# Optimization experiments

Hardware: AMD Instinct MI355X
Metric: run time of the kernel (lower is better)

The kernel has to match this reference:

```python
import jax, jax.numpy as jnp
import numpy as np

B, S, D = 16, 1024, 512
H = 2048
E = 16
TOP_K = 4


def setup_inputs() -> dict:
    key = jax.random.key(0)
    ks = jax.random.split(key, 8)
    scale = 0.02
    x = jax.random.normal(ks[0], (B, S, D), dtype=jnp.float32)
    router_w = jax.random.normal(ks[1], (D, E), dtype=jnp.float32) * scale
    router_b = jax.random.normal(ks[2], (E,), dtype=jnp.float32) * scale
    w1 = jax.random.normal(ks[3], (E, D, H), dtype=jnp.float32) * scale
    b1 = jax.random.normal(ks[4], (E, H), dtype=jnp.float32) * scale
    w2 = jax.random.normal(ks[5], (E, H, D), dtype=jnp.float32) * scale
    b2 = jax.random.normal(ks[6], (E, D), dtype=jnp.float32) * scale
    return {"x": x, "router_w": router_w, "router_b": router_b,
            "w1": w1, "b1": b1, "w2": w2, "b2": b2}


def reference(x, router_w, router_b, w1, b1, w2, b2):
    # x: [B, S, D] -> flatten tokens
    x_flat = x.reshape(-1, D)                       # [T, D]
    logits = x_flat @ router_w + router_b           # [T, E]
    top_vals, top_idx = jax.lax.top_k(logits, TOP_K)  # [T, K]
    gates = jax.nn.softmax(top_vals, axis=-1)       # softmax over selected experts only
    # Combined per-expert gate weight per token: sum over k slots routed to e.
    onehot = jax.nn.one_hot(top_idx, E, dtype=x.dtype)  # [T, K, E]
    comb = jnp.einsum('tk,tke->te', gates, onehot)      # [T, E]
    out = jnp.zeros_like(x_flat)
    for e in range(E):  # fixed small expert count
        h = jax.nn.relu(x_flat @ w1[e] + b1[e])     # [T, H]
        y = h @ w2[e] + b2[e]                       # [T, D]
        out = out + comb[:, e:e + 1] * y
    return out.reshape(x.shape)
```

## Files before the change

kernel.cpp:

```cpp
#include <hip/hip_runtime.h>
#include <stdint.h>

#define T_TOK 16384
#define DIM 512
#define HID 2048
#define NE 16
#define TOPK 4
#define BM 256
#define BN 256
#define BKT 64
#define PAIR_CAP 69632
#define MAX_TILES 272
#define NB_CNT 64
#define QOFF 2080

typedef short s8v __attribute__((ext_vector_type(8)));
typedef float f4v __attribute__((ext_vector_type(4)));
typedef unsigned int u4v __attribute__((ext_vector_type(4)));

__device__ __forceinline__ unsigned short f2bf(float f) {
  unsigned int u = __builtin_bit_cast(unsigned int, f);
  u = (u + 0x7fffu + ((u >> 16) & 1u)) >> 16;
  return (unsigned short)u;
}
__device__ __forceinline__ float bf2f(unsigned short h) {
  return __builtin_bit_cast(float, (unsigned int)h << 16);
}

__device__ __forceinline__ void gload16(const void* g, void* l) {
  __builtin_amdgcn_global_load_lds(
      (const __attribute__((address_space(1))) unsigned int*)(uintptr_t)g,
      (__attribute__((address_space(3))) unsigned int*)(uintptr_t)l,
      16, 0, 0);
}

__global__ __launch_bounds__(256) void k_transpose_cast(const float* __restrict__ src,
                                                        unsigned short* __restrict__ dst,
                                                        int R, int C) {
  __shared__ float tile[32][33];
  size_t zo = (size_t)blockIdx.z * R * C;
  src += zo; dst += zo;
  int c0 = blockIdx.x * 32, r0 = blockIdx.y * 32;
  int tx = threadIdx.x, ty = threadIdx.y;
#pragma unroll
  for (int i = 0; i < 4; ++i)
    tile[ty + 8 * i][tx] = src[(size_t)(r0 + ty + 8 * i) * C + c0 + tx];
  __syncthreads();
#pragma unroll
  for (int i = 0; i < 4; ++i)
    dst[(size_t)(c0 + ty + 8 * i) * R + r0 + tx] = f2bf(tile[tx][ty + 8 * i]);
}

__global__ __launch_bounds__(256) void k_router(const float* __restrict__ x,
                                                const float* __restrict__ rw,
                                                const float* __restrict__ rb,
                                                int* __restrict__ topki,
                                                float* __restrict__ topkg,
                                                unsigned short* __restrict__ xb) {
  int wv = threadIdx.x >> 6, lane = threadIdx.x & 63;
  int t = blockIdx.x * 4 + wv;
  const float* xr = x + (size_t)t * DIM;
  unsigned short* xbr = xb + (size_t)t * DIM;
  double acc[NE];
#pragma unroll
  for (int e = 0; e < NE; ++e) acc[e] = 0.0;
  for (int it = 0; it < DIM / 64; ++it) {
    float xv = xr[it * 64 + lane];
    xbr[it * 64 + lane] = f2bf(xv);
    const float* r = rw + (size_t)(it * 64 + lane) * NE;
#pragma unroll
    for (int e = 0; e < NE; ++e) acc[e] += (double)xv * (double)r[e];
  }
#pragma unroll
  for (int off = 32; off >= 1; off >>= 1) {
#pragma unroll
    for (int e = 0; e < NE; ++e) acc[e] += __shfl_xor(acc[e], off, 64);
  }
  if (lane == 0) {
    float v[NE];
#pragma unroll
    for (int e = 0; e < NE; ++e) v[e] = (float)acc[e] + rb[e];
    int idx[TOPK]; float val[TOPK];
#pragma unroll
    for (int k = 0; k < TOPK; ++k) {
      float best = -1e30f; int bi = 0;
#pragma unroll
      for (int e = 0; e < NE; ++e)
        if (v[e] > best) { best = v[e]; bi = e; }
      idx[k] = bi; val[k] = best; v[bi] = -1e30f;
    }
    float m = val[0], s = 0.f, g[TOPK];
#pragma unroll
    for (int k = 0; k < TOPK; ++k) { g[k] = __expf(val[k] - m); s += g[k]; }
    float inv = 1.f / s;
#pragma unroll
    for (int k = 0; k < TOPK; ++k) {
      topki[t * TOPK + k] = idx[k];
      topkg[t * TOPK + k] = g[k] * inv;
    }
  }
}

__global__ __launch_bounds__(256) void k_count(const int* __restrict__ topki,
                                               int* __restrict__ meta) {
  __shared__ int lcnt[NE];
  int tid = threadIdx.x;
  if (tid < NE) lcnt[tid] = 0;
  __syncthreads();
  int base = blockIdx.x * 1024 + tid * 4;
#pragma unroll
  for (int j = 0; j < 4; ++j) atomicAdd(&lcnt[topki[base + j]], 1);
  __syncthreads();
  if (tid < NE) meta[1056 + blockIdx.x * NE + tid] = lcnt[tid];
}

__global__ __launch_bounds__(256) void k_plan(int* __restrict__ meta,
                                              int* __restrict__ ptok,
                                              float* __restrict__ pgate) {
  __shared__ int cnt_s[NE], po_s[NE + 1];
  int tid = threadIdx.x;
  for (int i = tid; i < 1024; i += 256) meta[QOFF + i] = 0;
  if (tid < NE) {
    int s = 0;
    for (int b = 0; b < NB_CNT; ++b) s += meta[1056 + b * NE + tid];
    cnt_s[tid] = s;
  }
  __syncthreads();
  if (tid == 0) {
    int off = 0;
    for (int e = 0; e < NE; ++e) {
      po_s[e] = off;
      meta[1 + e] = off;
      off += ((cnt_s[e] + BM - 1) / BM) * BM;
    }
    po_s[NE] = off;
    meta[1 + NE] = off;
    meta[0] = off / BM;
  }
  __syncthreads();
  if (tid < NE) {
    int run = po_s[tid];
    for (int b = 0; b < NB_CNT; ++b) {
      meta[32 + b * NE + tid] = run;
      run += meta[1056 + b * NE + tid];
    }
  }
  for (int e = 0; e < NE; ++e) {
    int start = po_s[e] + cnt_s[e], end = po_s[e + 1];
    for (int i = start + tid; i < end; i += 256) { ptok[i] = 0; pgate[i] = 0.f; }
  }
}

__global__ __launch_bounds__(256) void k_scatter(const int* __restrict__ topki,
                                                 const float* __restrict__ topkg,
                                                 const int* __restrict__ meta,
                                                 int* __restrict__ ptok,
                                                 float* __restrict__ pgate,
                                                 int* __restrict__ sinv) {
  __shared__ int lcnt[NE];
  int tid = threadIdx.x;
  if (tid < NE) lcnt[tid] = 0;
  __syncthreads();
  int base = blockIdx.x * 1024 + tid * 4;
#pragma unroll
  for (int j = 0; j < 4; ++j) {
    int i = base + j;
    int e = topki[i];
    int r = atomicAdd(&lcnt[e], 1);
    int slot = meta[32 + blockIdx.x * NE + e] + r;
    ptok[slot] = i >> 2;
    pgate[slot] = topkg[i];
    sinv[i] = slot;
  }
}


#define EBAR() asm volatile("s_barrier" ::: "memory")
#define SP1() __builtin_amdgcn_s_setprio(1)
#define SP0() __builtin_amdgcn_s_setprio(0)
#define VMC(n) asm volatile("s_waitcnt vmcnt(" #n ")" ::: "memory")
#define NOP ((void)0)

#define STG(rg, kt, c) do {                                                            \
    int _k = (kt) * BKT;                                                               \
    if ((rg) < 2) {                                                                    \
      gload16(aP[rg][0] + _k, (char*)&Al[c][0] + (rg) * 16384 + w * 1024);             \
      gload16(aP[rg][1] + _k, (char*)&Al[c][0] + (rg) * 16384 + 8192 + w * 1024);      \
    } else {                                                                           \
      gload16(bP[(rg) - 2][0] + _k, (char*)&Bl[c][0] + ((rg) - 2) * 16384 + w * 1024); \
      gload16(bP[(rg) - 2][1] + _k, (char*)&Bl[c][0] + ((rg) - 2) * 16384 + 8192 + w * 1024); \
    }                                                                                  \
  } while (0)

#define RDA(c, mq) do {                                                                \
    _Pragma("unroll")                                                                  \
    for (int mt = 0; mt < 4; ++mt) {                                                   \
      af[mt][0] = __builtin_bit_cast(s8v, *(const u4v*)&Al[c][(mq) * 8192 + aoff + mt * 1024 + cs0]); \
      af[mt][1] = __builtin_bit_cast(s8v, *(const u4v*)&Al[c][(mq) * 8192 + aoff + mt * 1024 + cs1]); \
    }                                                                                  \
  } while (0)

#define RDB(c, nq) do {                                                                \
    _Pragma("unroll")                                                                  \
    for (int nt = 0; nt < 2; ++nt) {                                                   \
      bfr[nq][nt][0] = __builtin_bit_cast(s8v, *(const u4v*)&Bl[c][(nq) * 8192 + boff + nt * 1024 + cs0]); \
      bfr[nq][nt][1] = __builtin_bit_cast(s8v, *(const u4v*)&Bl[c][(nq) * 8192 + boff + nt * 1024 + cs1]); \
    }                                                                                  \
  } while (0)

#define MMQ(mq, nq) do {                                                               \
    _Pragma("unroll")                                                                  \
    for (int mt = 0; mt < 4; ++mt) {                                                   \
      _Pragma("unroll")                                                                \
      for (int nt = 0; nt < 2; ++nt) {                                                 \
        acc[(mq) * 4 + mt][(nq) * 2 + nt] = __builtin_amdgcn_mfma_f32_16x16x32_bf16(   \
            af[mt][0], bfr[nq][nt][0], acc[(mq) * 4 + mt][(nq) * 2 + nt], 0, 0, 0);    \
        acc[(mq) * 4 + mt][(nq) * 2 + nt] = __builtin_amdgcn_mfma_f32_16x16x32_bf16(   \
            af[mt][1], bfr[nq][nt][1], acc[(mq) * 4 + mt][(nq) * 2 + nt], 0, 0, 0);    \
      }                                                                                \
    }                                                                                  \
  } while (0)

#define FIRE(mq, nq) do { SP1(); MMQ(mq, nq); SP0(); } while (0)

__global__ __launch_bounds__(512, 2) void k_pipe(const unsigned short* xb,
                                                 const unsigned short* w1t,
                                                 const float* b1,
                                                 const unsigned short* w2t,
                                                 const float* b2,
                                                 const int* ptok,
                                                 const float* pgate,
                                                 const int* meta,
                                                 int* qctr,
                                                 unsigned short* hdst,
                                                 const unsigned short* hsrc,
                                                 unsigned short* yslot,
                                                 float* out,
                                                 int c1, int c2, int C) {
  __shared__ __align__(16) unsigned short Al[2][BM * BKT];
  __shared__ __align__(16) unsigned short Bl[2][BN * BKT];
  __shared__ int sh_item;
  int tid = threadIdx.x;
  int lane = tid & 63, w = tid >> 6;
  int wm = w >> 2, wn = w & 3;
  int lrow = lane & 15, quad = lane >> 4;
  int r7 = lrow & 7;
  int sub = lane >> 3, lg = (lane & 7) ^ sub;

  int aoff = (wm * 64 + lrow) * BKT;
  int boff = (wn * 32 + lrow) * BKT;
  int cs0 = (quad ^ r7) * 8;
  int cs1 = ((4 + quad) ^ r7) * 8;

  int T = meta[0];
  int t2 = 0, t1 = 0;
  if (c2 >= 0) { t2 = T - c2 * C; t2 = t2 < 0 ? 0 : (t2 > C ? C : t2); }
  if (c1 >= 0) { t1 = T - c1 * C; t1 = t1 < 0 ? 0 : (t1 > C ? C : t1); }
  int n2 = 2 * t2, nit = n2 + 8 * t1;

  for (;;) {
    if (tid == 0) sh_item = atomicAdd(qctr, 1);
    __syncthreads();
    int it = sh_item;
    if (it >= nit) break;

    bool g2 = it < n2;
    int tloc, nb, tile;
    if (g2) { tloc = it >> 1; nb = (it & 1) * BN; tile = c2 * C + tloc; }
    else { int j = it - n2; tloc = j >> 3; nb = (j & 7) * BN; tile = c1 * C + tloc; }
    int row0 = tile * BM;
    int e = 0;
#pragma unroll
    for (int i2 = 1; i2 < NE; ++i2)
      if (row0 >= meta[1 + i2]) e = i2;

    const unsigned short* aP[2][2];
    const unsigned short* bP[2][2];
    int NKT;
    if (!g2) {
      NKT = DIM / BKT;
#pragma unroll
      for (int h = 0; h < 2; ++h)
#pragma unroll
        for (int t = 0; t < 2; ++t) {
          int r = h * 128 + t * 64 + w * 8 + sub;
          aP[h][t] = xb + (size_t)ptok[row0 + r] * DIM + lg * 8;
          bP[h][t] = w1t + ((size_t)e * HID + nb + r) * DIM + lg * 8;
        }
    } else {
      NKT = HID / BKT;
#pragma unroll
      for (int h = 0; h < 2; ++h)
#pragma unroll
        for (int t = 0; t < 2; ++t) {
          int r = h * 128 + t * 64 + w * 8 + sub;
          aP[h][t] = hsrc + ((size_t)tloc * BM + r) * HID + lg * 8;
          bP[h][t] = w2t + ((size_t)e * DIM + nb + r) * HID + lg * 8;
        }
    }

    f4v acc[8][4] = {};
    s8v af[4][2];
    s8v bfr[2][2][2];

    STG(0, 0, 0); STG(2, 0, 0); STG(3, 0, 0); STG(1, 0, 0);
    STG(0, 1, 1); STG(2, 1, 1); STG(3, 1, 1);
    VMC(4);
    EBAR();

    int NI = NKT >> 1;
    for (int i = 0; i < NI - 1; ++i) {
      int bt = 2 * i;
      RDA(0, 0); RDB(0, 0); RDB(0, 1); STG(1, bt + 1, 1);
      FIRE(0, 0); EBAR();
      STG(0, bt + 2, 0);
      FIRE(0, 1); EBAR();
      RDA(0, 1); STG(2, bt + 2, 0);
      FIRE(1, 0); EBAR();
      STG(3, bt + 2, 0);
      FIRE(1, 1); VMC(6); EBAR();
      RDA(1, 0); RDB(1, 0); RDB(1, 1); STG(1, bt + 2, 0);
      FIRE(0, 0); EBAR();
      STG(0, bt + 3, 1);
      FIRE(0, 1); EBAR();
      RDA(1, 1); STG(2, bt + 3, 1);
      FIRE(1, 0); EBAR();
      STG(3, bt + 3, 1);
      FIRE(1, 1); VMC(6); EBAR();
    }
    {
      int bt = NKT - 2;
      RDA(0, 0); RDB(0, 0); RDB(0, 1); STG(1, bt + 1, 1);
      FIRE(0, 0); EBAR();
      FIRE(0, 1); EBAR();
      RDA(0, 1);
      FIRE(1, 0); EBAR();
      FIRE(1, 1); VMC(4); EBAR();
      RDA(1, 0); RDB(1, 0);
      FIRE(0, 0); VMC(2); EBAR();
      RDB(1, 1);
      FIRE(0, 1); VMC(0); EBAR();
      RDA(1, 1);
      FIRE(1, 0); EBAR();
      FIRE(1, 1); EBAR();
    }

    if (!g2) {
      size_t hrow0 = (size_t)tloc * BM;
      float bias[2][2];
#pragma unroll
      for (int nq = 0; nq < 2; ++nq)
#pragma unroll
        for (int nt = 0; nt < 2; ++nt)
          bias[nq][nt] = b1[e * HID + nb + nq * 128 + wn * 32 + nt * 16 + lrow];
#pragma unroll
      for (int mq = 0; mq < 2; ++mq) {
#pragma unroll
        for (int mt = 0; mt < 4; ++mt) {
#pragma unroll
          for (int j = 0; j < 4; ++j) {
            int grow = mq * 128 + wm * 64 + mt * 16 + quad * 4 + j;
            unsigned short* hr = hdst + (hrow0 + grow) * HID + nb + wn * 32 + lrow;
#pragma unroll
            for (int nq = 0; nq < 2; ++nq)
#pragma unroll
              for (int nt = 0; nt < 2; ++nt) {
                float v = acc[mq * 4 + mt][nq * 2 + nt][j] + bias[nq][nt];
                hr[nq * 128 + nt * 16] = f2bf(v > 0.f ? v : 0.f);
              }
          }
        }
      }
    } else {
      float bias[2][2];
#pragma unroll
      for (int nq = 0; nq < 2; ++nq)
#pragma unroll
        for (int nt = 0; nt < 2; ++nt)
          bias[nq][nt] = b2[e * DIM + nb + nq * 128 + wn * 32 + nt * 16 + lrow];
      if (yslot) {
#pragma unroll
        for (int mq = 0; mq < 2; ++mq) {
#pragma unroll
          for (int mt = 0; mt < 4; ++mt) {
#pragma unroll
            for (int j = 0; j < 4; ++j) {
              int p = row0 + mq * 128 + wm * 64 + mt * 16 + quad * 4 + j;
              float g = pgate[p];
              unsigned short* yr = yslot + (size_t)p * DIM + nb + wn * 32 + lrow;
#pragma unroll
              for (int nq = 0; nq < 2; ++nq)
#pragma unroll
                for (int nt = 0; nt < 2; ++nt)
                  yr[nq * 128 + nt * 16] = f2bf(g * (acc[mq * 4 + mt][nq * 2 + nt][j] + bias[nq][nt]));
            }
          }
        }
      } else {
#pragma unroll
        for (int mq = 0; mq < 2; ++mq) {
#pragma unroll
          for (int mt = 0; mt < 4; ++mt) {
#pragma unroll
            for (int j = 0; j < 4; ++j) {
              int p = row0 + mq * 128 + wm * 64 + mt * 16 + quad * 4 + j;
              float g = pgate[p];
              if (g != 0.f) {
                int tok = ptok[p];
                float* orow = out + (size_t)tok * DIM + nb + wn * 32 + lrow;
#pragma unroll
                for (int nq = 0; nq < 2; ++nq)
#pragma unroll
                  for (int nt = 0; nt < 2; ++nt)
                    atomicAdd(orow + nq * 128 + nt * 16, g * (acc[mq * 4 + mt][nq * 2 + nt][j] + bias[nq][nt]));
              }
            }
          }
        }
      }
    }
  }
}

__global__ __launch_bounds__(256) void k_gather(const unsigned short* __restrict__ yslot,
                                                const int* __restrict__ sinv,
                                                float* __restrict__ out) {
  int id = blockIdx.x * 256 + threadIdx.x;
  int t = id >> 7, d4 = (id & 127) << 2;
  int4 s = *(const int4*)(sinv + t * 4);
  int sl[4] = {s.x, s.y, s.z, s.w};
  float sum0 = 0.f, sum1 = 0.f, sum2 = 0.f, sum3 = 0.f;
#pragma unroll
  for (int k = 0; k < 4; ++k) {
    ushort4 v = *(const ushort4*)(yslot + (size_t)sl[k] * DIM + d4);
    sum0 += bf2f(v.x); sum1 += bf2f(v.y); sum2 += bf2f(v.z); sum3 += bf2f(v.w);
  }
  float4 r; r.x = sum0; r.y = sum1; r.z = sum2; r.w = sum3;
  *(float4*)(out + (size_t)t * DIM + d4) = r;
}

extern "C" void kernel_launch(void* const* d_in, const int* in_sizes, int n_in,
                              void* d_out, int out_size, void* d_ws, size_t ws_size,
                              hipStream_t stream) {
  const float* x  = (const float*)d_in[0];
  const float* rw = (const float*)d_in[1];
  const float* rb = (const float*)d_in[2];
  const float* w1 = (const float*)d_in[3];
  const float* b1 = (const float*)d_in[4];
  const float* w2 = (const float*)d_in[5];
  const float* b2 = (const float*)d_in[6];
  float* out = (float*)d_out;
  char* ws = (char*)d_ws;

  size_t o_xb    = 0;
  size_t o_w1t   = o_xb    + (size_t)T_TOK * DIM * 2;
  size_t o_w2t   = o_w1t   + (size_t)NE * DIM * HID * 2;
  size_t o_topki = o_w2t   + (size_t)NE * DIM * HID * 2;
  size_t o_topkg = o_topki + (size_t)T_TOK * TOPK * 4;
  size_t o_meta  = o_topkg + (size_t)T_TOK * TOPK * 4;
  size_t o_ptok  = o_meta  + 16384;
  size_t o_pgate = o_ptok  + (size_t)PAIR_CAP * 4;
  size_t o_sinv  = o_pgate + (size_t)PAIR_CAP * 4;
  size_t o_yslot = o_sinv  + (size_t)T_TOK * TOPK * 4;
  size_t o_hb    = o_yslot + (size_t)PAIR_CAP * DIM * 2;

  unsigned short* xb   = (unsigned short*)(ws + o_xb);
  unsigned short* w1t  = (unsigned short*)(ws + o_w1t);
  unsigned short* w2t  = (unsigned short*)(ws + o_w2t);
  int*            tki  = (int*)(ws + o_topki);
  float*          tkg  = (float*)(ws + o_topkg);
  int*            meta = (int*)(ws + o_meta);
  int*            ptok = (int*)(ws + o_ptok);
  float*          pgt  = (float*)(ws + o_pgate);
  int*            sinv = (int*)(ws + o_sinv);

  size_t tile_h = (size_t)BM * HID * 2;
  size_t avail = ws_size > o_hb ? ws_size - o_hb : 0;
  long Cd = (long)(avail / (2 * tile_h));
  int use_slot = Cd >= 1;

  k_router<<<T_TOK / 4, 256, 0, stream>>>(x, rw, rb, tki, tkg, xb);
  k_transpose_cast<<<dim3(HID / 32, DIM / 32, NE), dim3(32, 8), 0, stream>>>(w1, w1t, DIM, HID);
  k_transpose_cast<<<dim3(DIM / 32, HID / 32, NE), dim3(32, 8), 0, stream>>>(w2, w2t, HID, DIM);
  k_count<<<NB_CNT, 256, 0, stream>>>(tki, meta);
  k_plan<<<1, 256, 0, stream>>>(meta, ptok, pgt);
  k_scatter<<<NB_CNT, 256, 0, stream>>>(tki, tkg, meta, ptok, pgt, sinv);

  if (use_slot) {
    unsigned short* ysl = (unsigned short*)(ws + o_yslot);
    int C = (int)(Cd > MAX_TILES ? MAX_TILES : Cd);
    int n_chunks = (MAX_TILES + C - 1) / C;
    unsigned short* hb0 = (unsigned short*)(ws + o_hb);
    unsigned short* hb1 = hb0 + (size_t)C * BM * HID;
    for (int i = 0; i <= n_chunks; ++i) {
      unsigned short* dst = (i & 1) ? hb1 : hb0;
      unsigned short* src = (i & 1) ? hb0 : hb1;
      int c1 = (i < n_chunks) ? i : -1;
      int c2 = i - 1;
      k_pipe<<<256, 512, 0, stream>>>(xb, w1t, b1, w2t, b2, ptok, pgt, meta,
                                      meta + QOFF + i, dst, src, ysl, out, c1, c2, C);
    }
    k_gather<<<T_TOK * DIM / 4 / 256, 256, 0, stream>>>(ysl, sinv, out);
  } else {
    long Cf = (long)((ws_size - o_yslot) / tile_h);
    int C = (int)(Cf < 1 ? 1 : (Cf > MAX_TILES ? MAX_TILES : Cf));
    int n_chunks = (MAX_TILES + C - 1) / C;
    unsigned short* hb = (unsigned short*)(ws + o_yslot);
    hipMemsetAsync(d_out, 0, (size_t)T_TOK * DIM * 4, stream);
    for (int i = 0; i < n_chunks; ++i) {
      k_pipe<<<256, 512, 0, stream>>>(xb, w1t, b1, w2t, b2, ptok, pgt, meta,
                                      meta + QOFF + 2 * i, hb, hb, nullptr, out, i, -1, C);
      k_pipe<<<256, 512, 0, stream>>>(xb, w1t, b1, w2t, b2, ptok, pgt, meta,
                                      meta + QOFF + 2 * i + 1, hb, hb, nullptr, out, -1, i, C);
    }
  }
}
```

Measured before the change: 618.7 us.

## Split GEMM2 into 256x128 tiles and transpose MFMA operands for vector stores

The second GEMM (h @ w2) now uses 256x128 output tiles instead of 256x256, doubling its work items and using a dedicated pipeline with a single B half-tile. This improves load balance and parallelism for the long K=2048 loop. Both GEMMs swap the MFMA operand order so each lane holds four consecutive output columns, which lets epilogues use packed ushort4 stores and f4v bias loads instead of scalar strided stores. In exchange, GEMM2 loses some A-tile reuse per item, and the epilogue layout and code size change.

```diff
diff --git a/kernel.cpp b/kernel.cpp
--- a/kernel.cpp
+++ b/kernel.cpp
@@ -179,17 +179,18 @@
 #define SP1() __builtin_amdgcn_s_setprio(1)
 #define SP0() __builtin_amdgcn_s_setprio(0)
 #define VMC(n) asm volatile("s_waitcnt vmcnt(" #n ")" ::: "memory")
-#define NOP ((void)0)
-
-#define STG(rg, kt, c) do {                                                            \
-    int _k = (kt) * BKT;                                                               \
-    if ((rg) < 2) {                                                                    \
-      gload16(aP[rg][0] + _k, (char*)&Al[c][0] + (rg) * 16384 + w * 1024);             \
-      gload16(aP[rg][1] + _k, (char*)&Al[c][0] + (rg) * 16384 + 8192 + w * 1024);      \
-    } else {                                                                           \
-      gload16(bP[(rg) - 2][0] + _k, (char*)&Bl[c][0] + ((rg) - 2) * 16384 + w * 1024); \
-      gload16(bP[(rg) - 2][1] + _k, (char*)&Bl[c][0] + ((rg) - 2) * 16384 + 8192 + w * 1024); \
-    }                                                                                  \
+
+#define STGA(h, kt, c) do { int _k = (kt) * BKT;                                   \
+    gload16(aP[h][0] + _k, (char*)&Al[c][0] + (h) * 16384 + w * 1024);             \
+    gload16(aP[h][1] + _k, (char*)&Al[c][0] + (h) * 16384 + 8192 + w * 1024);      \
+  } while (0)
+#define STGB(nqr, kt, c) do { int _k = (kt) * BKT;                                 \
+    gload16(bP[nqr][0] + _k, (char*)&Bl[c][0] + (nqr) * 16384 + w * 1024);         \
+    gload16(bP[nqr][1] + _k, (char*)&Bl[c][0] + (nqr) * 16384 + 8192 + w * 1024);  \
+  } while (0)
+#define STGB2(kt, c) do { int _k = (kt) * BKT;                                     \
+    gload16(bP2[0] + _k, (char*)&Bl[c][0] + w * 1024);                             \
+    gload16(bP2[1] + _k, (char*)&Bl[c][0] + 8192 + w * 1024);                      \
   } while (0)
 
 #define RDA(c, mq) do {                                                                \
@@ -208,20 +209,42 @@
     }                                                                                  \
   } while (0)
 
-#define MMQ(mq, nq) do {                                                               \
+#define RDB2(c) do {                                                                   \
+    _Pragma("unroll")                                                                  \
+    for (int nt = 0; nt < 2; ++nt) {                                                   \
+      bfr[nt][0] = __builtin_bit_cast(s8v, *(const u4v*)&Bl[c][boff + nt * 1024 + cs0]); \
+      bfr[nt][1] = __builtin_bit_cast(s8v, *(const u4v*)&Bl[c][boff + nt * 1024 + cs1]); \
+    }                                                                                  \
+  } while (0)
+
+#define MMQ1(mq, nq) do {                                                              \
     _Pragma("unroll")                                                                  \
     for (int mt = 0; mt < 4; ++mt) {                                                   \
       _Pragma("unroll")                                                                \
       for (int nt = 0; nt < 2; ++nt) {                                                 \
-        acc[(mq) * 4 + mt][(nq) * 2 + nt] = __builtin_amdgcn_mfma_f32_16x16x32_bf16(   \
-            af[mt][0], bfr[nq][nt][0], acc[(mq) * 4 + mt][(nq) * 2 + nt], 0, 0, 0);    \
-        acc[(mq) * 4 + mt][(nq) * 2 + nt] = __builtin_amdgcn_mfma_f32_16x16x32_bf16(   \
-            af[mt][1], bfr[nq][nt][1], acc[(mq) * 4 + mt][(nq) * 2 + nt], 0, 0, 0);    \
+        acc[(nq) * 2 + nt][(mq) * 4 + mt] = __builtin_amdgcn_mfma_f32_16x16x32_bf16(   \
+            bfr[nq][nt][0], af[mt][0], acc[(nq) * 2 + nt][(mq) * 4 + mt], 0, 0, 0);    \
+        acc[(nq) * 2 + nt][(mq) * 4 + mt] = __builtin_amdgcn_mfma_f32_16x16x32_bf16(   \
+            bfr[nq][nt][1], af[mt][1], acc[(nq) * 2 + nt][(mq) * 4 + mt], 0, 0, 0);    \
       }                                                                                \
     }                                                                                  \
   } while (0)
 
-#define FIRE(mq, nq) do { SP1(); MMQ(mq, nq); SP0(); } while (0)
+#define MMQ2(mq) do {                                                                  \
+    _Pragma("unroll")                                                                  \
+    for (int mt = 0; mt < 4; ++mt) {                                                   \
+      _Pragma("unroll")                                                                \
+      for (int nt = 0; nt < 2; ++nt) {                                                 \
+        acc[nt][(mq) * 4 + mt] = __builtin_amdgcn_mfma_f32_16x16x32_bf16(              \
+            bfr[nt][0], af[mt][0], acc[nt][(mq) * 4 + mt], 0, 0, 0);                   \
+        acc[nt][(mq) * 4 + mt] = __builtin_amdgcn_mfma_f32_16x16x32_bf16(              \
+            bfr[nt][1], af[mt][1], acc[nt][(mq) * 4 + mt], 0, 0, 0);                   \
+      }                                                                                \
+    }                                                                                  \
+  } while (0)
+
+#define FIRE1(mq, nq) do { SP1(); MMQ1(mq, nq); SP0(); } while (0)
+#define FIRE2(mq) do { SP1(); MMQ2(mq); SP0(); } while (0)
 
 __global__ __launch_bounds__(512, 2) void k_pipe(const unsigned short* xb,
                                                  const unsigned short* w1t,
@@ -256,7 +279,7 @@
   int t2 = 0, t1 = 0;
   if (c2 >= 0) { t2 = T - c2 * C; t2 = t2 < 0 ? 0 : (t2 > C ? C : t2); }
   if (c1 >= 0) { t1 = T - c1 * C; t1 = t1 < 0 ? 0 : (t1 > C ? C : t1); }
-  int n2 = 2 * t2, nit = n2 + 8 * t1;
+  int n2 = 4 * t2, nit = n2 + 8 * t1;
 
   for (;;) {
     if (tid == 0) sh_item = atomicAdd(qctr, 1);
@@ -264,21 +287,116 @@
     int it = sh_item;
     if (it >= nit) break;
 
-    bool g2 = it < n2;
-    int tloc, nb, tile;
-    if (g2) { tloc = it >> 1; nb = (it & 1) * BN; tile = c2 * C + tloc; }
-    else { int j = it - n2; tloc = j >> 3; nb = (j & 7) * BN; tile = c1 * C + tloc; }
-    int row0 = tile * BM;
-    int e = 0;
-#pragma unroll
-    for (int i2 = 1; i2 < NE; ++i2)
-      if (row0 >= meta[1 + i2]) e = i2;
-
-    const unsigned short* aP[2][2];
-    const unsigned short* bP[2][2];
-    int NKT;
-    if (!g2) {
-      NKT = DIM / BKT;
+    if (it < n2) {
+      int tloc = it >> 2, nb = (it & 3) * 128;
+      int tile = c2 * C + tloc;
+      int row0 = tile * BM;
+      int e = 0;
+#pragma unroll
+      for (int i2 = 1; i2 < NE; ++i2)
+        if (row0 >= meta[1 + i2]) e = i2;
+
+      const unsigned short* aP[2][2];
+      const unsigned short* bP2[2];
+#pragma unroll
+      for (int h = 0; h < 2; ++h)
+#pragma unroll
+        for (int t = 0; t < 2; ++t)
+          aP[h][t] = hsrc + ((size_t)tloc * BM + h * 128 + t * 64 + w * 8 + sub) * HID + lg * 8;
+#pragma unroll
+      for (int t = 0; t < 2; ++t)
+        bP2[t] = w2t + ((size_t)e * DIM + nb + t * 64 + w * 8 + sub) * HID + lg * 8;
+
+      f4v acc[2][8] = {};
+      s8v af[4][2];
+      s8v bfr[2][2];
+
+      STGA(0, 0, 0); STGB2(0, 0); STGA(1, 0, 0);
+      STGA(0, 1, 1); STGB2(1, 1);
+      VMC(6);
+      EBAR();
+
+      const int NI = HID / BKT / 2;
+      for (int i = 0; i < NI - 1; ++i) {
+        int bt = 2 * i;
+        RDA(0, 0); RDB2(0); STGA(1, bt + 1, 1);
+        FIRE2(0); VMC(6); EBAR();
+        RDA(0, 1); STGA(0, bt + 2, 0); STGB2(bt + 2, 0);
+        FIRE2(1); VMC(6); EBAR();
+        RDA(1, 0); RDB2(1); STGA(1, bt + 2, 0);
+        FIRE2(0); VMC(6); EBAR();
+        RDA(1, 1); STGA(0, bt + 3, 1); STGB2(bt + 3, 1);
+        FIRE2(1); VMC(6); EBAR();
+      }
+      {
+        int bt = HID / BKT - 2;
+        RDA(0, 0); RDB2(0); STGA(1, bt + 1, 1);
+        FIRE2(0); VMC(6); EBAR();
+        RDA(0, 1);
+        FIRE2(1); VMC(2); EBAR();
+        RDA(1, 0); RDB2(1);
+        FIRE2(0); VMC(0); EBAR();
+        RDA(1, 1);
+        FIRE2(1); EBAR();
+      }
+
+      f4v bb[2];
+#pragma unroll
+      for (int nt = 0; nt < 2; ++nt)
+        bb[nt] = *(const f4v*)&b2[e * DIM + nb + wn * 32 + nt * 16 + quad * 4];
+      if (yslot) {
+#pragma unroll
+        for (int mq = 0; mq < 2; ++mq) {
+#pragma unroll
+          for (int mt = 0; mt < 4; ++mt) {
+            int trow = mq * 128 + wm * 64 + mt * 16 + lrow;
+            int p = row0 + trow;
+            float g = pgate[p];
+            unsigned short* yr = yslot + (size_t)p * DIM + nb + wn * 32 + quad * 4;
+#pragma unroll
+            for (int nt = 0; nt < 2; ++nt) {
+              f4v a = acc[nt][mq * 4 + mt];
+              ushort4 pk;
+              pk.x = f2bf(g * (a[0] + bb[nt][0]));
+              pk.y = f2bf(g * (a[1] + bb[nt][1]));
+              pk.z = f2bf(g * (a[2] + bb[nt][2]));
+              pk.w = f2bf(g * (a[3] + bb[nt][3]));
+              *(ushort4*)(yr + nt * 16) = pk;
+            }
+          }
+        }
+      } else {
+#pragma unroll
+        for (int mq = 0; mq < 2; ++mq) {
+#pragma unroll
+          for (int mt = 0; mt < 4; ++mt) {
+            int trow = mq * 128 + wm * 64 + mt * 16 + lrow;
+            int p = row0 + trow;
+            float g = pgate[p];
+            if (g != 0.f) {
+              int tok = ptok[p];
+              float* orow = out + (size_t)tok * DIM + nb + wn * 32 + quad * 4;
+#pragma unroll
+              for (int nt = 0; nt < 2; ++nt)
+#pragma unroll
+                for (int j = 0; j < 4; ++j)
+                  atomicAdd(orow + nt * 16 + j, g * (acc[nt][mq * 4 + mt][j] + bb[nt][j]));
+            }
+          }
+        }
+      }
+    } else {
+      int jj = it - n2;
+      int tloc = jj >> 3, nb = (jj & 7) * BN;
+      int tile = c1 * C + tloc;
+      int row0 = tile * BM;
+      int e = 0;
+#pragma unroll
+      for (int i2 = 1; i2 < NE; ++i2)
+        if (row0 >= meta[1 + i2]) e = i2;
+
+      const unsigned short* aP[2][2];
+      const unsigned short* bP[2][2];
 #pragma unroll
       for (int h = 0; h < 2; ++h)
 #pragma unroll
@@ -287,135 +405,82 @@
           aP[h][t] = xb + (size_t)ptok[row0 + r] * DIM + lg * 8;
           bP[h][t] = w1t + ((size_t)e * HID + nb + r) * DIM + lg * 8;
         }
-    } else {
-      NKT = HID / BKT;
-#pragma unroll
-      for (int h = 0; h < 2; ++h)
-#pragma unroll
-        for (int t = 0; t < 2; ++t) {
-          int r = h * 128 + t * 64 + w * 8 + sub;
-          aP[h][t] = hsrc + ((size_t)tloc * BM + r) * HID + lg * 8;
-          bP[h][t] = w2t + ((size_t)e * DIM + nb + r) * HID + lg * 8;
-        }
-    }
-
-    f4v acc[8][4] = {};
-    s8v af[4][2];
-    s8v bfr[2][2][2];
-
-    STG(0, 0, 0); STG(2, 0, 0); STG(3, 0, 0); STG(1, 0, 0);
-    STG(0, 1, 1); STG(2, 1, 1); STG(3, 1, 1);
-    VMC(4);
-    EBAR();
-
-    int NI = NKT >> 1;
-    for (int i = 0; i < NI - 1; ++i) {
-      int bt = 2 * i;
-      RDA(0, 0); RDB(0, 0); RDB(0, 1); STG(1, bt + 1, 1);
-      FIRE(0, 0); EBAR();
-      STG(0, bt + 2, 0);
-      FIRE(0, 1); EBAR();
-      RDA(0, 1); STG(2, bt + 2, 0);
-      FIRE(1, 0); EBAR();
-      STG(3, bt + 2, 0);
-      FIRE(1, 1); VMC(6); EBAR();
-      RDA(1, 0); RDB(1, 0); RDB(1, 1); STG(1, bt + 2, 0);
-      FIRE(0, 0); EBAR();
-      STG(0, bt + 3, 1);
-      FIRE(0, 1); EBAR();
-      RDA(1, 1); STG(2, bt + 3, 1);
-      FIRE(1, 0); EBAR();
-      STG(3, bt + 3, 1);
-      FIRE(1, 1); VMC(6); EBAR();
-    }
-    {
-      int bt = NKT - 2;
-      RDA(0, 0); RDB(0, 0); RDB(0, 1); STG(1, bt + 1, 1);
-      FIRE(0, 0); EBAR();
-      FIRE(0, 1); EBAR();
-      RDA(0, 1);
-      FIRE(1, 0); EBAR();
-      FIRE(1, 1); VMC(4); EBAR();
-      RDA(1, 0); RDB(1, 0);
-      FIRE(0, 0); VMC(2); EBAR();
-      RDB(1, 1);
-      FIRE(0, 1); VMC(0); EBAR();
-      RDA(1, 1);
-      FIRE(1, 0); EBAR();
-      FIRE(1, 1); EBAR();
-    }
-
-    if (!g2) {
+
+      f4v acc[4][8] = {};
+      s8v af[4][2];
+      s8v bfr[2][2][2];
+
+      STGA(0, 0, 0); STGB(0, 0, 0); STGB(1, 0, 0); STGA(1, 0, 0);
+      STGA(0, 1, 1); STGB(0, 1, 1); STGB(1, 1, 1);
+      VMC(4);
+      EBAR();
+
+      const int NI = DIM / BKT / 2;
+      for (int i = 0; i < NI - 1; ++i) {
+        int bt = 2 * i;
+        RDA(0, 0); RDB(0, 0); RDB(0, 1); STGA(1, bt + 1, 1);
+        FIRE1(0, 0); EBAR();
+        STGA(0, bt + 2, 0);
+        FIRE1(0, 1); EBAR();
+        RDA(0, 1); STGB(0, bt + 2, 0);
+        FIRE1(1, 0); EBAR();
+        STGB(1, bt + 2, 0);
+        FIRE1(1, 1); VMC(6); EBAR();
+        RDA(1, 0); RDB(1, 0); RDB(1, 1); STGA(1, bt + 2, 0);
+        FIRE1(0, 0); EBAR();
+        STGA(0, bt + 3, 1);
+        FIRE1(0, 1); EBAR();
+        RDA(1, 1); STGB(0, bt + 3, 1);
+        FIRE1(1, 0); EBAR();
+        STGB(1, bt + 3, 1);
+        FIRE1(1, 1); VMC(6); EBAR();
+      }
+      {
+        int bt = DIM / BKT - 2;
+        RDA(0, 0); RDB(0, 0); RDB(0, 1); STGA(1, bt + 1, 1);
+        FIRE1(0, 0); EBAR();
+        FIRE1(0, 1); EBAR();
+        RDA(0, 1);
+        FIRE1(1, 0); EBAR();
+        FIRE1(1, 1); VMC(4); EBAR();
+        RDA(1, 0); RDB(1, 0);
+        FIRE1(0, 0); VMC(2); EBAR();
+        RDB(1, 1);
+        FIRE1(0, 1); VMC(0); EBAR();
+        RDA(1, 1);
+        FIRE1(1, 0); EBAR();
+        FIRE1(1, 1); EBAR();
+      }
+
       size_t hrow0 = (size_t)tloc * BM;
-      float bias[2][2];
+      f4v bb[2][2];
 #pragma unroll
       for (int nq = 0; nq < 2; ++nq)
 #pragma unroll
         for (int nt = 0; nt < 2; ++nt)
-          bias[nq][nt] = b1[e * HID + nb + nq * 128 + wn * 32 + nt * 16 + lrow];
+          bb[nq][nt] = *(const f4v*)&b1[e * HID + nb + nq * 128 + wn * 32 + nt * 16 + quad * 4];
 #pragma unroll
       for (int mq = 0; mq < 2; ++mq) {
 #pragma unroll
         for (int mt = 0; mt < 4; ++mt) {
-#pragma unroll
-          for (int j = 0; j < 4; ++j) {
-            int grow = mq * 128 + wm * 64 + mt * 16 + quad * 4 + j;
-            unsigned short* hr = hdst + (hrow0 + grow) * HID + nb + wn * 32 + lrow;
-#pragma unroll
-            for (int nq = 0; nq < 2; ++nq)
-#pragma unroll
-              for (int nt = 0; nt < 2; ++nt) {
-                float v = acc[mq * 4 + mt][nq * 2 + nt][j] + bias[nq][nt];
-                hr[nq * 128 + nt * 16] = f2bf(v > 0.f ? v : 0.f);
-              }
-          }
-        }
-      }
-    } else {
-      float bias[2][2];
-#pragma unroll
-      for (int nq = 0; nq < 2; ++nq)
-#pragma unroll
-        for (int nt = 0; nt < 2; ++nt)
-          bias[nq][nt] = b2[e * DIM + nb + nq * 128 + wn * 32 + nt * 16 + lrow];
-      if (yslot) {
-#pragma unroll
-        for (int mq = 0; mq < 2; ++mq) {
-#pragma unroll
-          for (int mt = 0; mt < 4; ++mt) {
-#pragma unroll
-            for (int j = 0; j < 4; ++j) {
-              int p = row0 + mq * 128 + wm * 64 + mt * 16 + quad * 4 + j;
-              float g = pgate[p];
-              unsigned short* yr = yslot + (size_t)p * DIM + nb + wn * 32 + lrow;
-#pragma unroll
-              for (int nq = 0; nq < 2; ++nq)
-#pragma unroll
-                for (int nt = 0; nt < 2; ++nt)
-                  yr[nq * 128 + nt * 16] = f2bf(g * (acc[mq * 4 + mt][nq * 2 + nt][j] + bias[nq][nt]));
+          int trow = mq * 128 + wm * 64 + mt * 16 + lrow;
+          unsigned short* hr = hdst + (hrow0 + trow) * HID + nb + wn * 32 + quad * 4;
+#pragma unroll
+          for (int nq = 0; nq < 2; ++nq)
+#pragma unroll
+            for (int nt = 0; nt < 2; ++nt) {
+              f4v a = acc[nq * 2 + nt][mq * 4 + mt];
+              ushort4 pk;
+              float v0 = a[0] + bb[nq][nt][0];
+              float v1 = a[1] + bb[nq][nt][1];
+              float v2 = a[2] + bb[nq][nt][2];
+              float v3 = a[3] + bb[nq][nt][3];
+              pk.x = f2bf(v0 > 0.f ? v0 : 0.f);
+              pk.y = f2bf(v1 > 0.f ? v1 : 0.f);
+              pk.z = f2bf(v2 > 0.f ? v2 : 0.f);
+              pk.w = f2bf(v3 > 0.f ? v3 : 0.f);
+              *(ushort4*)(hr + nq * 128 + nt * 16) = pk;
             }
-          }
-        }
-      } else {
-#pragma unroll
-        for (int mq = 0; mq < 2; ++mq) {
-#pragma unroll
-          for (int mt = 0; mt < 4; ++mt) {
-#pragma unroll
-            for (int j = 0; j < 4; ++j) {
-              int p = row0 + mq * 128 + wm * 64 + mt * 16 + quad * 4 + j;
-              float g = pgate[p];
-              if (g != 0.f) {
-                int tok = ptok[p];
-                float* orow = out + (size_t)tok * DIM + nb + wn * 32 + lrow;
-#pragma unroll
-                for (int nq = 0; nq < 2; ++nq)
-#pragma unroll
-                  for (int nt = 0; nt < 2; ++nt)
-                    atomicAdd(orow + nq * 128 + nt * 16, g * (acc[mq * 4 + mt][nq * 2 + nt][j] + bias[nq][nt]));
-              }
-            }
-          }
         }
       }
     }
```

Measured after the change: 662.6 us. 1.07x slower.
